# Performance work log

Hardware: AMD Instinct MI355X
Metric: run time of the kernel (lower is better)

Reference implementation:

```python
import jax, jax.numpy as jnp
import numpy as np

B, S, D, H = 2, 2048, 1024, 16
DK = D // H


def setup_inputs() -> dict:
    key = jax.random.key(0)
    ks = jax.random.split(key, 13)
    std = 1.0 / np.sqrt(D)
    inp = {
        "query": jax.random.normal(ks[0], (B, S, D), jnp.float32),
        "key": jax.random.normal(ks[1], (B, S, D), jnp.float32),
        "value": jax.random.normal(ks[2], (B, S, D), jnp.float32),
        "mask": jax.random.randint(ks[3], (B, S, S), 0, 2, jnp.int32),
        "Wq": jax.random.normal(ks[4], (D, D), jnp.float32) * std,
        "bq": jax.random.normal(ks[5], (D,), jnp.float32) * std,
        "Wk": jax.random.normal(ks[6], (D, D), jnp.float32) * std,
        "bk": jax.random.normal(ks[7], (D,), jnp.float32) * std,
        "Wv": jax.random.normal(ks[8], (D, D), jnp.float32) * std,
        "bv": jax.random.normal(ks[9], (D,), jnp.float32) * std,
        "Wo": jax.random.normal(ks[10], (D, D), jnp.float32) * std,
        "bo": jax.random.normal(ks[11], (D,), jnp.float32) * std,
    }
    return inp


def reference(query, key, value, mask, Wq, bq, Wk, bk, Wv, bv, Wo, bo):
    # QKV projections (torch Linear: x @ W.T + b), then split heads -> [B,H,S,DK]
    def proj(x, W, b):
        return (x @ W.T + b).reshape(B, S, H, DK).transpose(0, 2, 1, 3)

    q = proj(query, Wq, bq)
    k = proj(key, Wk, bk)
    v = proj(value, Wv, bv)

    scores = jnp.einsum("bhqd,bhkd->bhqk", q, k) / np.sqrt(DK)
    # mask [B,S,S] broadcast over heads; masked_fill(mask==0, -1e9)
    scores = jnp.where(mask[:, None, :, :] == 0, jnp.float32(-1e9), scores)
    p_attn = jax.nn.softmax(scores, axis=-1)
    x = jnp.einsum("bhqk,bhkd->bhqd", p_attn, v)
    x = x.transpose(0, 2, 1, 3).reshape(B, S, D)
    return x @ Wo.T + bo
```

## Files before the change

kernel.cpp:

```cpp
#include <hip/hip_runtime.h>
#include <hip/hip_bf16.h>
#include <cstdint>
#include <cstddef>

#define NB 2
#define NS 2048
#define ND 1024
#define NH 16
#define NDK 64
#define NT (NS / 64)

typedef __attribute__((ext_vector_type(4))) float f32x4;
typedef __attribute__((ext_vector_type(8))) short bf16x8;

#define MFMA_16x16x32_BF16(a,b,c) __builtin_amdgcn_mfma_f32_16x16x32_bf16((a),(b),(c),0,0,0)

__device__ __forceinline__ uint16_t f2bf(float f){
  uint32_t u = __float_as_uint(f);
  u += 0x7fffu + ((u >> 16) & 1u);
  return (uint16_t)(u >> 16);
}
__device__ __forceinline__ uint32_t bfpack2(float a, float b){
  uint32_t r;
  asm volatile("v_cvt_pk_bf16_f32 %0, %1, %2" : "=v"(r) : "v"(a), "v"(b));
  return r;
}
__device__ __forceinline__ void gload_lds16(const void* g, void* l){
  __builtin_amdgcn_global_load_lds((const __attribute__((address_space(1))) void*)g,
                                   (__attribute__((address_space(3))) void*)l, 16, 0, 0);
}

__global__ void cvt3_f32_bf16(const float* __restrict__ a, const float* __restrict__ b2,
                              const float* __restrict__ c, uint16_t* __restrict__ oa,
                              uint16_t* __restrict__ ob, uint16_t* __restrict__ oc, int n8){
  const float* in = (blockIdx.y == 0) ? a : (blockIdx.y == 1) ? b2 : c;
  uint16_t* out   = (blockIdx.y == 0) ? oa : (blockIdx.y == 1) ? ob : oc;
  int i0 = blockIdx.x * blockDim.x + threadIdx.x;
  int stride = gridDim.x * blockDim.x;
  for(int i = i0; i < n8; i += stride){
    const float4* p = (const float4*)(in) + (size_t)i * 2;
    float4 x = p[0], y = p[1];
    bf16x8 o;
    o[0]=(short)f2bf(x.x); o[1]=(short)f2bf(x.y); o[2]=(short)f2bf(x.z); o[3]=(short)f2bf(x.w);
    o[4]=(short)f2bf(y.x); o[5]=(short)f2bf(y.y); o[6]=(short)f2bf(y.z); o[7]=(short)f2bf(y.w);
    *((bf16x8*)(out) + i) = o;
  }
}
__global__ void cvt4_f32_bf16(const float* __restrict__ a, const float* __restrict__ b2,
                              const float* __restrict__ c, const float* __restrict__ d,
                              uint16_t* __restrict__ oa, uint16_t* __restrict__ ob,
                              uint16_t* __restrict__ oc, uint16_t* __restrict__ od, int n8){
  const float* in = (blockIdx.y == 0) ? a : (blockIdx.y == 1) ? b2 : (blockIdx.y == 2) ? c : d;
  uint16_t* out   = (blockIdx.y == 0) ? oa : (blockIdx.y == 1) ? ob : (blockIdx.y == 2) ? oc : od;
  int i0 = blockIdx.x * blockDim.x + threadIdx.x;
  int stride = gridDim.x * blockDim.x;
  for(int i = i0; i < n8; i += stride){
    const float4* p = (const float4*)(in) + (size_t)i * 2;
    float4 x = p[0], y = p[1];
    bf16x8 o;
    o[0]=(short)f2bf(x.x); o[1]=(short)f2bf(x.y); o[2]=(short)f2bf(x.z); o[3]=(short)f2bf(x.w);
    o[4]=(short)f2bf(y.x); o[5]=(short)f2bf(y.y); o[6]=(short)f2bf(y.z); o[7]=(short)f2bf(y.w);
    *((bf16x8*)(out) + i) = o;
  }
}

__global__ void mask_bits(const int* __restrict__ mask, unsigned long long* __restrict__ bits, int nchunks){
  int wid  = (blockIdx.x * blockDim.x + threadIdx.x) >> 6;
  int lane = threadIdx.x & 63;
  int nw   = (gridDim.x * blockDim.x) >> 6;
  for(int c = wid; c < nchunks; c += nw){
    int mv = mask[(size_t)c * 64 + lane];
    unsigned long long bb = __ballot(mv != 0);
    if(lane == 0) bits[c] = bb;
  }
}

template<bool OUTF32>
__global__ __launch_bounds__(256, 4)
void gemm_bt(const uint16_t* __restrict__ A0, const uint16_t* __restrict__ A1, const uint16_t* __restrict__ A2,
             const uint16_t* __restrict__ W0, const uint16_t* __restrict__ W1, const uint16_t* __restrict__ W2,
             const float* __restrict__ b0, const float* __restrict__ b1, const float* __restrict__ b2,
             void* __restrict__ C0, void* __restrict__ C1, void* __restrict__ C2,
             int M, int N, int K, int vtz)
{
  const int z = blockIdx.z;
  const uint16_t* A   = (z == 0) ? A0 : (z == 1) ? A1 : A2;
  const uint16_t* W   = (z == 0) ? W0 : (z == 1) ? W1 : W2;
  const float*   bias = (z == 0) ? b0 : (z == 1) ? b1 : b2;
  void*          Cout = (z == 0) ? C0 : (z == 1) ? C1 : C2;

  __shared__ __align__(16) uint16_t Asm[128 * 64];
  __shared__ __align__(16) uint16_t Bsm[128 * 64];

  const int t = threadIdx.x;
  const int lane = t & 63, w = t >> 6;
  const int l15 = lane & 15, g = lane >> 4;
  const int bm = blockIdx.y * 128, bn = blockIdx.x * 128;
  const int wr = (w >> 1) * 64, wc = (w & 1) * 64;

  f32x4 acc[4][4] = {};

  const int srow = lane >> 3;
  const int schk = (lane & 7) ^ srow;

  const uint16_t* gA = A + (size_t)(bm + w * 32 + srow) * K + schk * 8;
  const uint16_t* gB = W + (size_t)(bn + w * 32 + srow) * K + schk * 8;
  uint16_t* lA = &Asm[(w * 32) * 64];
  uint16_t* lB = &Bsm[(w * 32) * 64];

  const int xr = l15 & 7;
  int aOff[2][4], bOff[2][4];
  #pragma unroll
  for(int kk = 0; kk < 2; ++kk)
    #pragma unroll
    for(int m = 0; m < 4; ++m){
      aOff[kk][m] = (wr + m*16 + l15) * 64 + (((kk*4 + g) ^ xr) << 3);
      bOff[kk][m] = (wc + m*16 + l15) * 64 + (((kk*4 + g) ^ xr) << 3);
    }

  for(int k0 = 0; k0 < K; k0 += 64){
    #pragma unroll
    for(int j = 0; j < 4; ++j){
      gload_lds16(gA + (size_t)(8 * j) * K, lA + (8 * j) * 64);
      gload_lds16(gB + (size_t)(8 * j) * K, lB + (8 * j) * 64);
    }
    gA += 64; gB += 64;
    __syncthreads();
    #pragma unroll
    for(int kk = 0; kk < 2; ++kk){
      bf16x8 af[4], bfr[4];
      #pragma unroll
      for(int m = 0; m < 4; ++m) af[m]  = *(const bf16x8*)&Asm[aOff[kk][m]];
      #pragma unroll
      for(int n = 0; n < 4; ++n) bfr[n] = *(const bf16x8*)&Bsm[bOff[kk][n]];
      #pragma unroll
      for(int m = 0; m < 4; ++m)
        #pragma unroll
        for(int n = 0; n < 4; ++n)
          acc[m][n] = MFMA_16x16x32_BF16(af[m], bfr[n], acc[m][n]);
    }
    __syncthreads();
  }

  if(z == vtz){
    uint16_t* Vt = (uint16_t*)Cout;
    #pragma unroll
    for(int m = 0; m < 4; ++m){
      const int row = bm + wr + m*16 + g*4;
      const int bb = row >> 11, ss = row & (NS - 1);
      #pragma unroll
      for(int n = 0; n < 4; ++n){
        const int col = bn + wc + n*16 + l15;
        const float bv = bias[col];
        float v0 = acc[m][n][0] + bv, v1 = acc[m][n][1] + bv;
        float v2 = acc[m][n][2] + bv, v3 = acc[m][n][3] + bv;
        uint2 pk; pk.x = bfpack2(v0, v1); pk.y = bfpack2(v2, v3);
        size_t dst = ((size_t)(bb * NH + (col >> 6)) * NDK + (col & 63)) * NS + ss;
        *(uint2*)&Vt[dst] = pk;
      }
    }
  } else {
    #pragma unroll
    for(int m = 0; m < 4; ++m){
      const int row = bm + wr + m*16 + g*4;
      #pragma unroll
      for(int n = 0; n < 4; ++n){
        const int col = bn + wc + n*16 + l15;
        const float bv = bias[col];
        #pragma unroll
        for(int j = 0; j < 4; ++j){
          float v = acc[m][n][j] + bv;
          if (OUTF32) ((float*)Cout)[(size_t)(row + j) * N + col] = v;
          else        ((uint16_t*)Cout)[(size_t)(row + j) * N + col] = f2bf(v);
        }
      }
    }
  }
}

__device__ __forceinline__ int swz64(int r, int chunk){
  return r * 64 + (((chunk) ^ (r & 7)) << 3);
}

__global__ __launch_bounds__(256, 4)
void attn_fwd(const uint16_t* __restrict__ Qp, const uint16_t* __restrict__ Kp,
              const uint16_t* __restrict__ Vtg, const uint2* __restrict__ Mbits,
              uint16_t* __restrict__ Xo)
{
  __shared__ __align__(16) uint16_t Ksm[2][64 * 64];
  __shared__ __align__(16) uint16_t Vtsm[2][64 * 64];
  __shared__ __align__(16) uint16_t Psm[4][16 * 64];

  const int t = threadIdx.x, lane = t & 63, w = t >> 6;
  const int l15 = lane & 15, g = lane >> 4;
  const int b = blockIdx.z, h = blockIdx.y, q0 = blockIdx.x * 64;
  const int qbase = q0 + w * 16;

  bf16x8 qf0, qf1;
  {
    const uint16_t* qptr = Qp + (size_t)(b * NS + qbase + l15) * ND + h * NDK + g * 8;
    qf0 = *(const bf16x8*)(qptr);
    qf1 = *(const bf16x8*)(qptr + 32);
  }

  bf16x8 ones;
  #pragma unroll
  for(int e = 0; e < 8; ++e) ones[e] = (short)0x3F80;

  f32x4 acc[4] = {};
  f32x4 acl = {};
  const float SCL = 0.125f * 1.44269504f;
  const float MC  = 23.0831f;

  const int srow = lane >> 3;
  const int schk = (lane & 7) ^ srow;

  const uint16_t* gK0 = Kp + (size_t)(b * NS + w * 16 + srow) * ND + h * NDK + schk * 8;
  const uint16_t* gK1 = gK0 + 8 * ND;
  const uint16_t* gV0 = Vtg + (size_t)(b * NH + h) * NDK * NS + (size_t)(w * 16 + srow) * NS + schk * 8;
  const uint16_t* gV1 = gV0 + 8 * NS;

  uint16_t* lK = &Ksm[0][(w * 16) * 64];
  uint16_t* lV = &Vtsm[0][(w * 16) * 64];

  int kOffA[4], kOffB[4], vOff[2][4];
  #pragma unroll
  for(int i = 0; i < 4; ++i){
    kOffA[i] = swz64(i * 16 + l15, g);
    kOffB[i] = swz64(i * 16 + l15, g + 4);
  }
  #pragma unroll
  for(int c2 = 0; c2 < 2; ++c2)
    #pragma unroll
    for(int tt = 0; tt < 4; ++tt)
      vOff[c2][tt] = swz64(tt * 16 + l15, c2 * 4 + g);
  const int xorw = (l15 & 7) << 3;
  const int prow = l15 * 64;
  int pW[4], pR[2];
  #pragma unroll
  for(int i = 0; i < 4; ++i) pW[i] = prow + ((16 * i + g * 4) ^ xorw);
  #pragma unroll
  for(int c2 = 0; c2 < 2; ++c2) pR[c2] = prow + ((c2 * 32 + g * 8) ^ xorw);
  uint16_t* PsmW = Psm[w];

  const uint2* Mptr = Mbits + (size_t)(b * NS + qbase + l15) * (NS / 64);

  gload_lds16(gK0, lK);
  gload_lds16(gK1, lK + 8 * 64);
  gload_lds16(gV0, lV);
  gload_lds16(gV1, lV + 8 * 64);
  gK0 += 64 * ND; gK1 += 64 * ND; gV0 += 64; gV1 += 64;
  __syncthreads();

  int cur = 0;
  for(int ti = 0; ti < NT; ++ti){
    if(ti + 1 < NT){
      const int nc = (cur ^ 1) * 4096;
      gload_lds16(gK0, lK + nc);
      gload_lds16(gK1, lK + nc + 8 * 64);
      gload_lds16(gV0, lV + nc);
      gload_lds16(gV1, lV + nc + 8 * 64);
    }
    gK0 += 64 * ND; gK1 += 64 * ND; gV0 += 64; gV1 += 64;
    const uint2 mm = Mptr[ti];
    const uint16_t* Kc = &Ksm[0][cur * 4096];
    const uint16_t* Vc = &Vtsm[0][cur * 4096];

    f32x4 s4[4];
    __builtin_amdgcn_s_setprio(1);
    #pragma unroll
    for(int i = 0; i < 4; ++i){
      bf16x8 kf0 = *(const bf16x8*)&Kc[kOffA[i]];
      bf16x8 kf1 = *(const bf16x8*)&Kc[kOffB[i]];
      f32x4 zr = {};
      zr = MFMA_16x16x32_BF16(kf0, qf0, zr);
      zr = MFMA_16x16x32_BF16(kf1, qf1, zr);
      s4[i] = zr;
    }
    __builtin_amdgcn_s_setprio(0);

    const uint32_t w0 = mm.x >> (g * 4);
    const uint32_t w1 = mm.y >> (g * 4);
    #pragma unroll
    for(int i = 0; i < 4; ++i){
      const uint32_t ww = (i < 2) ? w0 : w1;
      #pragma unroll
      for(int j = 0; j < 4; ++j){
        const int bitpos = (i & 1) * 16 + j;
        float e = exp2f(fmaf(s4[i][j], SCL, -MC));
        uint32_t sm = (uint32_t)(((int)(ww << (31 - bitpos))) >> 31);
        s4[i][j] = __uint_as_float(sm & __float_as_uint(e));
      }
    }

    #pragma unroll
    for(int i = 0; i < 4; ++i){
      uint2 pk;
      pk.x = bfpack2(s4[i][0], s4[i][1]);
      pk.y = bfpack2(s4[i][2], s4[i][3]);
      *(uint2*)&PsmW[pW[i]] = pk;
    }

    __builtin_amdgcn_s_setprio(1);
    #pragma unroll
    for(int c2 = 0; c2 < 2; ++c2){
      bf16x8 pf = *(const bf16x8*)&PsmW[pR[c2]];
      acl = MFMA_16x16x32_BF16(pf, ones, acl);
      #pragma unroll
      for(int tt = 0; tt < 4; ++tt){
        bf16x8 vf = *(const bf16x8*)&Vc[vOff[c2][tt]];
        acc[tt] = MFMA_16x16x32_BF16(pf, vf, acc[tt]);
      }
    }
    __builtin_amdgcn_s_setprio(0);

    __syncthreads();
    cur ^= 1;
  }

  #pragma unroll
  for(int j = 0; j < 4; ++j){
    const float inv = 1.0f / acl[j];
    const int qr = qbase + g * 4 + j;
    #pragma unroll
    for(int tt = 0; tt < 4; ++tt)
      Xo[(size_t)(b * NS + qr) * ND + h * NDK + tt * 16 + l15] = f2bf(acc[tt][j] * inv);
  }
}

extern "C" void kernel_launch(void* const* d_in, const int* in_sizes, int n_in,
                              void* d_out, int out_size, void* d_ws, size_t ws_size,
                              hipStream_t stream)
{
  const float* query = (const float*)d_in[0];
  const float* key   = (const float*)d_in[1];
  const float* value = (const float*)d_in[2];
  const int*   mask  = (const int*)d_in[3];
  const float* Wq = (const float*)d_in[4];
  const float* bq = (const float*)d_in[5];
  const float* Wk = (const float*)d_in[6];
  const float* bk = (const float*)d_in[7];
  const float* Wv = (const float*)d_in[8];
  const float* bv = (const float*)d_in[9];
  const float* Wo = (const float*)d_in[10];
  const float* bo = (const float*)d_in[11];
  float* out = (float*)d_out;

  const size_t NX = (size_t)NB * NS * ND;
  const size_t NW = (size_t)ND * ND;

  uint16_t* ws  = (uint16_t*)d_ws;
  uint16_t* Xq  = ws;
  uint16_t* Xk  = Xq  + NX;
  uint16_t* Xv  = Xk  + NX;
  uint16_t* Wqb = Xv  + NX;
  uint16_t* Wkb = Wqb + NW;
  uint16_t* Wvb = Wkb + NW;
  uint16_t* Wob = Wvb + NW;
  uint16_t* Qp  = Wob + NW;
  uint16_t* Kp  = Qp  + NX;
  uint16_t* Vt  = Kp  + NX;
  uint16_t* Xa  = Vt  + NX;

  unsigned long long* Mb = (unsigned long long*)Xq;

  cvt3_f32_bf16<<<dim3(2048, 3), 256, 0, stream>>>(query, key, value, Xq, Xk, Xv, (int)(NX / 8));
  cvt4_f32_bf16<<<dim3(512, 4), 256, 0, stream>>>(Wq, Wk, Wv, Wo, Wqb, Wkb, Wvb, Wob, (int)(NW / 8));

  dim3 gproj(ND / 128, (NB * NS) / 128, 3);
  gemm_bt<false><<<gproj, 256, 0, stream>>>(Xq, Xk, Xv,
                                            Wqb, Wkb, Wvb,
                                            bq, bk, bv,
                                            (void*)Qp, (void*)Kp, (void*)Vt,
                                            NB * NS, ND, ND, 2);

  {
    int nchunks = (int)((size_t)NB * NS * NS / 64);
    mask_bits<<<2048, 256, 0, stream>>>(mask, Mb, nchunks);
  }

  attn_fwd<<<dim3(NS / 64, NH, NB), 256, 0, stream>>>(Qp, Kp, Vt, (const uint2*)Mb, Xa);

  dim3 gout(ND / 128, (NB * NS) / 128, 1);
  gemm_bt<true><<<gout, 256, 0, stream>>>(Xa, Xa, Xa,
                                          Wob, Wob, Wob,
                                          bo, bo, bo,
                                          (void*)out, (void*)out, (void*)out,
                                          NB * NS, ND, ND, -1);
}
```

Before: 163.7 us.

## Load K/V fragments directly from global into registers, drop LDS staging

Removes the double-buffered LDS staging of K and V tiles and the per-tile block barrier. Each wave now loads its K and V MFMA fragments straight from global memory (via cache) into registers every iteration. This cuts LDS traffic and synchronisation, but each of the four waves reloads the same K/V data, raising global/L2 traffic, and nothing prefetches across iterations, so load latency may be exposed.

```diff
diff --git a/kernel.cpp b/kernel.cpp
--- a/kernel.cpp
+++ b/kernel.cpp
@@ -178,17 +178,11 @@
   }
 }
 
-__device__ __forceinline__ int swz64(int r, int chunk){
-  return r * 64 + (((chunk) ^ (r & 7)) << 3);
-}
-
 __global__ __launch_bounds__(256, 4)
 void attn_fwd(const uint16_t* __restrict__ Qp, const uint16_t* __restrict__ Kp,
               const uint16_t* __restrict__ Vtg, const uint2* __restrict__ Mbits,
               uint16_t* __restrict__ Xo)
 {
-  __shared__ __align__(16) uint16_t Ksm[2][64 * 64];
-  __shared__ __align__(16) uint16_t Vtsm[2][64 * 64];
   __shared__ __align__(16) uint16_t Psm[4][16 * 64];
 
   const int t = threadIdx.x, lane = t & 63, w = t >> 6;
@@ -212,28 +206,10 @@
   const float SCL = 0.125f * 1.44269504f;
   const float MC  = 23.0831f;
 
-  const int srow = lane >> 3;
-  const int schk = (lane & 7) ^ srow;
-
-  const uint16_t* gK0 = Kp + (size_t)(b * NS + w * 16 + srow) * ND + h * NDK + schk * 8;
-  const uint16_t* gK1 = gK0 + 8 * ND;
-  const uint16_t* gV0 = Vtg + (size_t)(b * NH + h) * NDK * NS + (size_t)(w * 16 + srow) * NS + schk * 8;
-  const uint16_t* gV1 = gV0 + 8 * NS;
-
-  uint16_t* lK = &Ksm[0][(w * 16) * 64];
-  uint16_t* lV = &Vtsm[0][(w * 16) * 64];
-
-  int kOffA[4], kOffB[4], vOff[2][4];
-  #pragma unroll
-  for(int i = 0; i < 4; ++i){
-    kOffA[i] = swz64(i * 16 + l15, g);
-    kOffB[i] = swz64(i * 16 + l15, g + 4);
-  }
-  #pragma unroll
-  for(int c2 = 0; c2 < 2; ++c2)
-    #pragma unroll
-    for(int tt = 0; tt < 4; ++tt)
-      vOff[c2][tt] = swz64(tt * 16 + l15, c2 * 4 + g);
+  const uint16_t* pK0 = Kp  + (size_t)(b * NS + l15) * ND + h * NDK + g * 8;
+  const uint16_t* pV0 = Vtg + ((size_t)(b * NH + h) * NDK + l15) * NS + g * 8;
+  const uint2* Mptr = Mbits + (size_t)(b * NS + qbase + l15) * (NS / 64);
+
   const int xorw = (l15 & 7) << 3;
   const int prow = l15 * 64;
   int pW[4], pR[2];
@@ -243,38 +219,30 @@
   for(int c2 = 0; c2 < 2; ++c2) pR[c2] = prow + ((c2 * 32 + g * 8) ^ xorw);
   uint16_t* PsmW = Psm[w];
 
-  const uint2* Mptr = Mbits + (size_t)(b * NS + qbase + l15) * (NS / 64);
-
-  gload_lds16(gK0, lK);
-  gload_lds16(gK1, lK + 8 * 64);
-  gload_lds16(gV0, lV);
-  gload_lds16(gV1, lV + 8 * 64);
-  gK0 += 64 * ND; gK1 += 64 * ND; gV0 += 64; gV1 += 64;
-  __syncthreads();
-
-  int cur = 0;
   for(int ti = 0; ti < NT; ++ti){
-    if(ti + 1 < NT){
-      const int nc = (cur ^ 1) * 4096;
-      gload_lds16(gK0, lK + nc);
-      gload_lds16(gK1, lK + nc + 8 * 64);
-      gload_lds16(gV0, lV + nc);
-      gload_lds16(gV1, lV + nc + 8 * 64);
-    }
-    gK0 += 64 * ND; gK1 += 64 * ND; gV0 += 64; gV1 += 64;
+    bf16x8 kf[8], vf[8];
+    #pragma unroll
+    for(int i = 0; i < 4; ++i){
+      const uint16_t* p = pK0 + (size_t)(i * 16) * ND;
+      kf[2*i]   = *(const bf16x8*)(p);
+      kf[2*i+1] = *(const bf16x8*)(p + 32);
+    }
+    #pragma unroll
+    for(int tt = 0; tt < 4; ++tt){
+      const uint16_t* p = pV0 + (size_t)(tt * 16) * NS;
+      vf[tt]     = *(const bf16x8*)(p);
+      vf[4 + tt] = *(const bf16x8*)(p + 32);
+    }
     const uint2 mm = Mptr[ti];
-    const uint16_t* Kc = &Ksm[0][cur * 4096];
-    const uint16_t* Vc = &Vtsm[0][cur * 4096];
+    pK0 += 64 * ND; pV0 += 64;
 
     f32x4 s4[4];
     __builtin_amdgcn_s_setprio(1);
     #pragma unroll
     for(int i = 0; i < 4; ++i){
-      bf16x8 kf0 = *(const bf16x8*)&Kc[kOffA[i]];
-      bf16x8 kf1 = *(const bf16x8*)&Kc[kOffB[i]];
       f32x4 zr = {};
-      zr = MFMA_16x16x32_BF16(kf0, qf0, zr);
-      zr = MFMA_16x16x32_BF16(kf1, qf1, zr);
+      zr = MFMA_16x16x32_BF16(kf[2*i],   qf0, zr);
+      zr = MFMA_16x16x32_BF16(kf[2*i+1], qf1, zr);
       s4[i] = zr;
     }
     __builtin_amdgcn_s_setprio(0);
@@ -307,15 +275,10 @@
       bf16x8 pf = *(const bf16x8*)&PsmW[pR[c2]];
       acl = MFMA_16x16x32_BF16(pf, ones, acl);
       #pragma unroll
-      for(int tt = 0; tt < 4; ++tt){
-        bf16x8 vf = *(const bf16x8*)&Vc[vOff[c2][tt]];
-        acc[tt] = MFMA_16x16x32_BF16(pf, vf, acc[tt]);
-      }
+      for(int tt = 0; tt < 4; ++tt)
+        acc[tt] = MFMA_16x16x32_BF16(pf, vf[c2 * 4 + tt], acc[tt]);
     }
     __builtin_amdgcn_s_setprio(0);
-
-    __syncthreads();
-    cur ^= 1;
   }
 
   #pragma unroll
```

Result: slower. 326.1 us (+99.2%).

## Fuse mask bit-packing into input conversion and pipeline attention loads with split waitcnts

Applied to the files above, without the earlier changes.

The mask-to-bitmask pass moves into the input conversion kernel as an extra grid slice, removing one launch. Its output now goes to a dedicated workspace region past Xa, because it can no longer alias Xq while Xq is being written. In the attention loop, the mask word for the next tile is prefetched a step ahead. __syncthreads is replaced by an explicit vmcnt wait that leaves the next tile's loads outstanding, plus raw barriers, so global-to-LDS loads overlap compute. The hand-written vmcnt count depends on the exact order of issued loads, so a miscount could read incomplete data.

```diff
diff --git a/kernel.cpp b/kernel.cpp
--- a/kernel.cpp
+++ b/kernel.cpp
@@ -30,9 +30,22 @@
                                    (__attribute__((address_space(3))) void*)l, 16, 0, 0);
 }
 
-__global__ void cvt3_f32_bf16(const float* __restrict__ a, const float* __restrict__ b2,
-                              const float* __restrict__ c, uint16_t* __restrict__ oa,
-                              uint16_t* __restrict__ ob, uint16_t* __restrict__ oc, int n8){
+__global__ void prep_inputs(const float* __restrict__ a, const float* __restrict__ b2,
+                            const float* __restrict__ c, uint16_t* __restrict__ oa,
+                            uint16_t* __restrict__ ob, uint16_t* __restrict__ oc,
+                            const int* __restrict__ mask, unsigned long long* __restrict__ bits,
+                            int n8, int nchunks){
+  if(blockIdx.y == 3){
+    int wid  = (blockIdx.x * blockDim.x + threadIdx.x) >> 6;
+    int lane = threadIdx.x & 63;
+    int nw   = (gridDim.x * blockDim.x) >> 6;
+    for(int ch = wid; ch < nchunks; ch += nw){
+      int mv = mask[(size_t)ch * 64 + lane];
+      unsigned long long bb = __ballot(mv != 0);
+      if(lane == 0) bits[ch] = bb;
+    }
+    return;
+  }
   const float* in = (blockIdx.y == 0) ? a : (blockIdx.y == 1) ? b2 : c;
   uint16_t* out   = (blockIdx.y == 0) ? oa : (blockIdx.y == 1) ? ob : oc;
   int i0 = blockIdx.x * blockDim.x + threadIdx.x;
@@ -64,17 +77,6 @@
   }
 }
 
-__global__ void mask_bits(const int* __restrict__ mask, unsigned long long* __restrict__ bits, int nchunks){
-  int wid  = (blockIdx.x * blockDim.x + threadIdx.x) >> 6;
-  int lane = threadIdx.x & 63;
-  int nw   = (gridDim.x * blockDim.x) >> 6;
-  for(int c = wid; c < nchunks; c += nw){
-    int mv = mask[(size_t)c * 64 + lane];
-    unsigned long long bb = __ballot(mv != 0);
-    if(lane == 0) bits[c] = bb;
-  }
-}
-
 template<bool OUTF32>
 __global__ __launch_bounds__(256, 4)
 void gemm_bt(const uint16_t* __restrict__ A0, const uint16_t* __restrict__ A1, const uint16_t* __restrict__ A2,
@@ -249,20 +251,26 @@
   gload_lds16(gK1, lK + 8 * 64);
   gload_lds16(gV0, lV);
   gload_lds16(gV1, lV + 8 * 64);
+  uint2 mmc = Mptr[0];
   gK0 += 64 * ND; gK1 += 64 * ND; gV0 += 64; gV1 += 64;
-  __syncthreads();
 
   int cur = 0;
   for(int ti = 0; ti < NT; ++ti){
+    uint2 mmn;
     if(ti + 1 < NT){
       const int nc = (cur ^ 1) * 4096;
       gload_lds16(gK0, lK + nc);
       gload_lds16(gK1, lK + nc + 8 * 64);
       gload_lds16(gV0, lV + nc);
       gload_lds16(gV1, lV + nc + 8 * 64);
-    }
-    gK0 += 64 * ND; gK1 += 64 * ND; gV0 += 64; gV1 += 64;
-    const uint2 mm = Mptr[ti];
+      mmn = Mptr[ti + 1];
+      gK0 += 64 * ND; gK1 += 64 * ND; gV0 += 64; gV1 += 64;
+      asm volatile("s_waitcnt vmcnt(5)" ::: "memory");
+    } else {
+      asm volatile("s_waitcnt vmcnt(0)" ::: "memory");
+    }
+    __builtin_amdgcn_s_barrier();
+
     const uint16_t* Kc = &Ksm[0][cur * 4096];
     const uint16_t* Vc = &Vtsm[0][cur * 4096];
 
@@ -279,8 +287,8 @@
     }
     __builtin_amdgcn_s_setprio(0);
 
-    const uint32_t w0 = mm.x >> (g * 4);
-    const uint32_t w1 = mm.y >> (g * 4);
+    const uint32_t w0 = mmc.x >> (g * 4);
+    const uint32_t w1 = mmc.y >> (g * 4);
     #pragma unroll
     for(int i = 0; i < 4; ++i){
       const uint32_t ww = (i < 2) ? w0 : w1;
@@ -314,8 +322,10 @@
     }
     __builtin_amdgcn_s_setprio(0);
 
-    __syncthreads();
+    asm volatile("s_waitcnt lgkmcnt(0)" ::: "memory");
+    __builtin_amdgcn_s_barrier();
     cur ^= 1;
+    mmc = mmn;
   }
 
   #pragma unroll
@@ -361,10 +371,12 @@
   uint16_t* Kp  = Qp  + NX;
   uint16_t* Vt  = Kp  + NX;
   uint16_t* Xa  = Vt  + NX;
-
-  unsigned long long* Mb = (unsigned long long*)Xq;
-
-  cvt3_f32_bf16<<<dim3(2048, 3), 256, 0, stream>>>(query, key, value, Xq, Xk, Xv, (int)(NX / 8));
+  unsigned long long* Mb = (unsigned long long*)(Xa + NX);
+
+  const int nchunks = (int)((size_t)NB * NS * NS / 64);
+
+  prep_inputs<<<dim3(2048, 4), 256, 0, stream>>>(query, key, value, Xq, Xk, Xv,
+                                                 mask, Mb, (int)(NX / 8), nchunks);
   cvt4_f32_bf16<<<dim3(512, 4), 256, 0, stream>>>(Wq, Wk, Wv, Wo, Wqb, Wkb, Wvb, Wob, (int)(NW / 8));
 
   dim3 gproj(ND / 128, (NB * NS) / 128, 3);
@@ -374,11 +386,6 @@
                                             (void*)Qp, (void*)Kp, (void*)Vt,
                                             NB * NS, ND, ND, 2);
 
-  {
-    int nchunks = (int)((size_t)NB * NS * NS / 64);
-    mask_bits<<<2048, 256, 0, stream>>>(mask, Mb, nchunks);
-  }
-
   attn_fwd<<<dim3(NS / 64, NH, NB), 256, 0, stream>>>(Qp, Kp, Vt, (const uint2*)Mb, Xa);
 
   dim3 gout(ND / 128, (NB * NS) / 128, 1);
```

After: 160.8 us. About the same (-1.8%).
